# Optimization experiments

Measured on AMD Instinct MI355X. Metric: run time of the kernel, lower is better.

Reference implementation:

```python
import jax, jax.numpy as jnp
import numpy as np

B, T = 128, 100
DZ, DA, DU, K, DOBS, H = 64, 32, 8, 8, 16, 128
JITTER = 1e-4  # _safe_cholesky: sym + jitter*I, then first try adds 1.0*jitter*I again


def setup_inputs() -> dict:
    key = jax.random.key(0)
    ks = jax.random.split(key, 10)
    eye_z = jnp.eye(DZ, dtype=jnp.float32)
    # stable-ish per-component transition matrices
    A_mats = 0.9 * eye_z[None] + 0.05 * jax.random.normal(ks[0], (K, DZ, DZ), jnp.float32)
    B_mats = 0.1 * jax.random.normal(ks[1], (K, DZ, DU), jnp.float32)
    C_mats = 0.3 * jax.random.normal(ks[2], (K, DA, DZ), jnp.float32)
    a_seq = jax.random.normal(ks[3], (B, T, DA), jnp.float32)
    h_obs = jax.random.normal(ks[4], (B, DOBS), jnp.float32)
    u_seq = jax.random.normal(ks[5], (B, T, DU), jnp.float32)
    mask = jnp.ones((B, T), jnp.float32)
    a_0 = jnp.zeros((1, DA), jnp.float32)          # nn.Parameter a_0
    P_0 = 10.0 * eye_z                              # 10 * eye(dim_z)
    Q = 0.05 * eye_z                                # Q_std * eye(dim_z)
    R = 0.05 * jnp.eye(DA, dtype=jnp.float32)       # R_std * eye(dim_a)
    din = DA + DOBS + DU
    s = 1.0 / float(np.sqrt(H))
    W_ih = s * jax.random.normal(ks[6], (3 * H, din), jnp.float32)
    W_hh = s * jax.random.normal(ks[7], (3 * H, H), jnp.float32)
    b_ih = jnp.zeros((3 * H,), jnp.float32)
    b_hh = jnp.zeros((3 * H,), jnp.float32)
    W_out = s * jax.random.normal(ks[8], (K, H), jnp.float32)
    b_out = jnp.zeros((K,), jnp.float32)
    return dict(a_seq=a_seq, h_obs=h_obs, u_seq=u_seq, mask=mask,
                A_mats=A_mats, B_mats=B_mats, C_mats=C_mats,
                a_0=a_0, P_0=P_0, Q=Q, R=R,
                W_ih=W_ih, W_hh=W_hh, b_ih=b_ih, b_hh=b_hh,
                W_out=W_out, b_out=b_out, epoch=100)


def _sym(M):
    return 0.5 * (M + jnp.swapaxes(M, -1, -2))


def _gru_alpha(x, h, W_ih, W_hh, b_ih, b_hh, W_out, b_out):
    # GRU-cell alpha_net: mixture weights over K components
    gi = x @ W_ih.T + b_ih
    gh = h @ W_hh.T + b_hh
    ir, iz, inn = jnp.split(gi, 3, axis=-1)
    hr, hz, hn = jnp.split(gh, 3, axis=-1)
    r = jax.nn.sigmoid(ir + hr)
    zg = jax.nn.sigmoid(iz + hz)
    n = jnp.tanh(inn + r * hn)
    h_new = (1.0 - zg) * n + zg * h
    alpha = jax.nn.softmax(h_new @ W_out.T + b_out, axis=-1)
    return alpha, h_new


def _kalman_forward(a_seq, h_obs, u_seq, mask, A_mats, B_mats, C_mats,
                    a_0, P_0, Q, R, W_ih, W_hh, b_ih, b_hh, W_out, b_out):
    Bsz = a_seq.shape[0]
    I = jnp.eye(DZ, dtype=a_seq.dtype)

    def mix(alpha):
        A = jnp.einsum('bk,kij->bij', alpha, A_mats)
        Bc = jnp.einsum('bk,kij->bij', alpha, B_mats)
        C = jnp.einsum('bk,kij->bij', alpha, C_mats)
        return A, Bc, C

    def alpha_net(a, u, h):
        x = jnp.concatenate([a, h_obs, u], axis=-1)
        return _gru_alpha(x, h, W_ih, W_hh, b_ih, b_hh, W_out, b_out)

    gru_h = jnp.zeros((Bsz, H), a_seq.dtype)
    a_prev = jnp.broadcast_to(a_0, (Bsz, DA))
    alpha0, gru_h = alpha_net(a_prev, u_seq[:, 0], gru_h)
    A_k0, B_k0, C_k0 = mix(alpha0)

    z0 = jnp.zeros((Bsz, DZ), a_seq.dtype)
    P0 = jnp.broadcast_to(P_0, (Bsz, DZ, DZ))

    def step(carry, inp):
        z_prev, P, h, A_k, B_k, C_k = carry
        a_k, u_k, m_k = inp  # [B,da], [B,du], [B]
        mk = m_k[:, None]
        # predict with matrices chosen at previous step
        z = jnp.einsum('bij,bj->bi', A_k, z_prev) + jnp.einsum('bij,bj->bi', B_k, u_k)
        a_hat = jnp.einsum('bij,bj->bi', C_k, z)
        r_k = a_k - a_hat
        CP = jnp.einsum('bij,bjk->bik', C_k, P)                      # C P
        S = jnp.einsum('bik,bjk->bij', CP, C_k) + R                   # C P C^T + R
        # K = solve(S^T, C P^T)^T  (i.e. K = P C^T S^{-1})
        CPt = jnp.einsum('bij,bkj->bik', C_k, P)
        Kg = jnp.swapaxes(jnp.linalg.solve(jnp.swapaxes(S, -1, -2), CPt), -1, -2)
        Kg = Kg * m_k[:, None, None]
        IKC = I - jnp.einsum('bij,bjk->bik', Kg, C_k)
        # Joseph form update
        P_filt = (jnp.einsum('bij,bjk,blk->bil', IKC, P, IKC)
                  + jnp.einsum('bij,jk,blk->bil', Kg, R, Kg))
        P_filt = _sym(P_filt)
        z_mean = z + jnp.einsum('bij,bj->bi', Kg, r_k)
        L = jnp.linalg.cholesky(_sym(P_filt) + 2.0 * JITTER * I)      # safe cholesky
        z_filt = z_mean                                               # dist.mean
        a_filt = jnp.einsum('bij,bj->bi', C_k, z_filt)
        a_k_hat = mk * a_k + (1.0 - mk) * a_filt
        C_old = C_k
        alpha, h = alpha_net(a_k_hat, u_k, h)
        A_n, B_n, C_n = mix(alpha)
        z_pred = (jnp.einsum('bij,bj->bi', A_n, z_filt)
                  + jnp.einsum('bij,bj->bi', B_n, u_k))
        a_pred = jnp.einsum('bij,bj->bi', C_n, z_pred)
        P_pred = _sym(jnp.einsum('bij,bjk,blk->bil', A_n, P_filt, A_n) + Q)
        carry = (z_filt, P_pred, h, A_n, B_n, C_n)
        out = (z_filt, P_filt, z_pred, P_pred, alpha, a_filt, a_pred,
               S, z_mean, L, A_n, B_n, C_old)
        return carry, out

    xs = (jnp.swapaxes(a_seq, 0, 1), jnp.swapaxes(u_seq, 0, 1), jnp.swapaxes(mask, 0, 1))
    _, outs = jax.lax.scan(step, (z0, P0, gru_h, A_k0, B_k0, C_k0), xs)
    # scan outputs are [T, B, ...] -> [B, T, ...]
    (z_filt, P_filt, z_pred, P_pred, alpha_seq, a_filt, a_pred,
     S_pred, z_means, z_scale_tril, A_seq, B_seq, C_seq) = jax.tree.map(
        lambda x: jnp.swapaxes(x, 0, 1), outs)
    return (z_filt, P_filt, z_pred, a_filt, a_pred, P_pred, alpha_seq,
            A_seq, B_seq, C_seq, z_means, z_scale_tril, S_pred)


def reference(a_seq, h_obs, u_seq, mask, A_mats, B_mats, C_mats,
              a_0, P_0, Q, R, W_ih, W_hh, b_ih, b_hh, W_out, b_out, epoch):
    # epoch >= warmup/burn-in thresholds (all 0), so no detach branches apply
    return _kalman_forward(a_seq, h_obs, u_seq, mask, A_mats, B_mats, C_mats,
                           a_0, P_0, Q, R, W_ih, W_hh, b_ih, b_hh, W_out, b_out)
```

## Files before the change

### kernel.cpp

```cpp
#include <hip/hip_runtime.h>

typedef float f4 __attribute__((ext_vector_type(4)));

#define NT 256
#define BB 128
#define BT 100
#define DZc 64
#define DAc 32
#define DUc 8
#define KMIX 8
#define DOBSc 16
#define HG 128
#define DINc 56

#define O_ZFILT   0LL
#define O_PFILT   819200LL
#define O_ZPRED   53248000LL
#define O_AFILT   54067200LL
#define O_APRED   54476800LL
#define O_PPRED   54886400LL
#define O_ALPHA   107315200LL
#define O_ASEQ    107417600LL
#define O_BSEQ    159846400LL
#define O_CSEQ    166400000LL
#define O_ZMEAN   192614400LL
#define O_LTRIL   193433600LL
#define O_SPRED   245862400LL

__device__ __forceinline__ float dot4(f4 a, f4 b) {
    return a[0]*b[0] + a[1]*b[1] + a[2]*b[2] + a[3]*b[3];
}

struct SMem {
    float P[DZc][68];
    float A[DZc][68];
    float AT[DZc][68];
    float Wk[DZc][68];
    float Qm[DZc][68];
    float C[DAc][68];
    float CP[DAc][68];
    float Xm[DAc][68];
    float S[DAc][33];
    float Rm[DAc][33];
    float dinv[DAc];
    float Bm[DZc][8];
    float z[DZc], zp[DZc], zn[DZc];
    float h[HG];
    float gh[3*HG], gi[3*HG];
    float x[64];
    float ak[DAc], rvec[DAc];
    float u[8];
    float lg[8];
    float mk;
};

template<bool EMIT>
__device__ __forceinline__ void mix_apply(SMem& s, int tid, size_t bt, const float* al8,
    const float* __restrict__ A_mats, const float* __restrict__ B_mats,
    const float* __restrict__ C_mats, float* __restrict__ out)
{
    const f4* A4 = (const f4*)A_mats;
    const f4* B4 = (const f4*)B_mats;
    const f4* C4 = (const f4*)C_mats;
    #pragma unroll 2
    for (int e = 0; e < 4; ++e) {
        int i4 = tid + e*256;
        f4 acc = {0.f,0.f,0.f,0.f};
        #pragma unroll
        for (int k = 0; k < 8; ++k) acc += al8[k] * A4[k*1024 + i4];
        int row = i4 >> 4, cb = (i4 & 15) * 4;
        *(f4*)&s.A[row][cb] = acc;
        s.AT[cb][row] = acc[0]; s.AT[cb+1][row] = acc[1];
        s.AT[cb+2][row] = acc[2]; s.AT[cb+3][row] = acc[3];
        if (EMIT) *(f4*)&out[O_ASEQ + bt*4096 + (size_t)i4*4] = acc;
    }
    if (tid < 128) {
        int i4 = tid;
        f4 acc = {0.f,0.f,0.f,0.f};
        #pragma unroll
        for (int k = 0; k < 8; ++k) acc += al8[k] * B4[k*128 + i4];
        *(f4*)&s.Bm[i4>>1][(i4&1)*4] = acc;
        if (EMIT) *(f4*)&out[O_BSEQ + bt*512 + (size_t)i4*4] = acc;
    }
    #pragma unroll 1
    for (int e = 0; e < 2; ++e) {
        int i4 = tid + e*256;
        f4 acc = {0.f,0.f,0.f,0.f};
        #pragma unroll
        for (int k = 0; k < 8; ++k) acc += al8[k] * C4[k*512 + i4];
        *(f4*)&s.C[i4>>4][(i4&15)*4] = acc;
    }
}

__global__ void __launch_bounds__(NT, 1)
kalman_seq(const float* __restrict__ a_seq, const float* __restrict__ h_obs,
           const float* __restrict__ u_seq, const float* __restrict__ mask,
           const float* __restrict__ A_mats, const float* __restrict__ B_mats,
           const float* __restrict__ C_mats, const float* __restrict__ a_0,
           const float* __restrict__ P_0, const float* __restrict__ Q,
           const float* __restrict__ R, const float* __restrict__ W_ih,
           const float* __restrict__ W_hh, const float* __restrict__ b_ih,
           const float* __restrict__ b_hh, const float* __restrict__ W_out,
           const float* __restrict__ b_out, float* __restrict__ out)
{
    __shared__ SMem s;
    const int b = blockIdx.x;
    const int tid = threadIdx.x;
    const int r4 = (tid >> 4) << 2;
    const int c4 = (tid & 15) << 2;

    for (int idx = tid; idx < DZc*DZc; idx += NT) {
        s.P[idx >> 6][idx & 63]  = P_0[idx];
        s.Qm[idx >> 6][idx & 63] = Q[idx];
    }
    for (int idx = tid; idx < DAc*DAc; idx += NT) s.Rm[idx >> 5][idx & 31] = R[idx];
    if (tid < HG) s.h[tid] = 0.f;
    if (tid < DZc) s.z[tid] = 0.f;
    if (tid < DAc)                 s.x[tid] = a_0[tid];
    else if (tid < DAc + DOBSc)    s.x[tid] = h_obs[b*DOBSc + (tid - DAc)];
    else if (tid < DINc)           s.x[tid] = u_seq[(size_t)b*BT*DUc + (tid - DAc - DOBSc)];
    __syncthreads();

    for (int g = tid; g < 3*HG; g += NT) {
        const float* wi = W_ih + (size_t)g * DINc;
        f4 ai = {0.f,0.f,0.f,0.f};
        #pragma unroll 7
        for (int q = 0; q < 14; ++q) ai += *(const f4*)(wi + q*4) * *(const f4*)&s.x[q*4];
        s.gi[g] = ai[0]+ai[1]+ai[2]+ai[3] + b_ih[g];
        s.gh[g] = b_hh[g];
    }
    __syncthreads();
    if (tid < HG) {
        float r  = 1.f / (1.f + expf(-(s.gi[tid] + s.gh[tid])));
        float zg = 1.f / (1.f + expf(-(s.gi[HG+tid] + s.gh[HG+tid])));
        float n  = tanhf(s.gi[2*HG+tid] + r * s.gh[2*HG+tid]);
        s.h[tid] = (1.f - zg) * n;
    }
    __syncthreads();
    if (tid < KMIX) {
        const float* wo = W_out + tid * HG;
        f4 acc = {0.f,0.f,0.f,0.f};
        #pragma unroll 8
        for (int q = 0; q < 32; ++q) acc += *(const f4*)(wo + q*4) * *(const f4*)&s.h[q*4];
        s.lg[tid] = acc[0]+acc[1]+acc[2]+acc[3] + b_out[tid];
    }
    __syncthreads();
    {
        float lg[8];
        #pragma unroll
        for (int k = 0; k < 8; ++k) lg[k] = s.lg[k];
        float mx = lg[0];
        #pragma unroll
        for (int k = 1; k < 8; ++k) mx = fmaxf(mx, lg[k]);
        float al[8]; float sum = 0.f;
        #pragma unroll
        for (int k = 0; k < 8; ++k) { al[k] = expf(lg[k] - mx); sum += al[k]; }
        float rs = 1.f / sum;
        #pragma unroll
        for (int k = 0; k < 8; ++k) al[k] *= rs;
        mix_apply<false>(s, tid, 0, al, A_mats, B_mats, C_mats, out);
    }
    __syncthreads();

    for (int t = 0; t < BT; ++t) {
        const size_t bt = (size_t)b * BT + t;

        if (tid < 64) {
            float acc = 0.f;
            #pragma unroll 8
            for (int k = 0; k < DZc; ++k) acc += s.AT[k][tid] * s.z[k];
            const float* up = u_seq + bt*DUc;
            #pragma unroll
            for (int q = 0; q < DUc; ++q) acc += s.Bm[tid][q] * up[q];
            s.zp[tid] = acc;
        } else if (tid < 96) {
            float av = a_seq[bt*DAc + (tid-64)];
            s.ak[tid-64] = av;
            s.x[tid-64] = av;
        } else if (tid < 104) {
            float uv = u_seq[bt*DUc + (tid-96)];
            s.u[tid-96] = uv; s.x[48 + (tid-96)] = uv;
        } else if (tid == 104) {
            s.mk = mask[bt];
        }
        __syncthreads();
        const float mkv = s.mk;
        const bool mk1 = (mkv == 1.0f);

        {
            const int r = tid >> 3;
            const int c8 = (tid & 7) * 8;
            f4 acc0 = {0.f,0.f,0.f,0.f}, acc1 = {0.f,0.f,0.f,0.f};
            #pragma unroll 4
            for (int k4 = 0; k4 < 16; ++k4) {
                f4 cr = *(const f4*)&s.C[r][k4*4];
                #pragma unroll
                for (int kk = 0; kk < 4; ++kk) {
                    float cv = cr[kk];
                    acc0 += cv * *(const f4*)&s.P[k4*4+kk][c8];
                    acc1 += cv * *(const f4*)&s.P[k4*4+kk][c8+4];
                }
            }
            *(f4*)&s.CP[r][c8]   = acc0;
            *(f4*)&s.CP[r][c8+4] = acc1;
        }
        if (tid < DAc) {
            float acc = 0.f;
            #pragma unroll 4
            for (int k4 = 0; k4 < 16; ++k4)
                acc += dot4(*(const f4*)&s.C[tid][k4*4], *(const f4*)&s.zp[k4*4]);
            s.rvec[tid] = s.ak[tid] - acc;
        }
        __syncthreads();

        {
            const int r = tid >> 3;
            const int cb = (tid & 7) * 4;
            f4 acc = {0.f,0.f,0.f,0.f};
            #pragma unroll 4
            for (int k4 = 0; k4 < 16; ++k4) {
                f4 a = *(const f4*)&s.CP[r][k4*4];
                #pragma unroll
                for (int j = 0; j < 4; ++j)
                    acc[j] += dot4(a, *(const f4*)&s.C[cb+j][k4*4]);
            }
            f4 rm = {s.Rm[r][cb], s.Rm[r][cb+1], s.Rm[r][cb+2], s.Rm[r][cb+3]};
            f4 v = acc + rm;
            s.S[r][cb] = v[0]; s.S[r][cb+1] = v[1]; s.S[r][cb+2] = v[2]; s.S[r][cb+3] = v[3];
            *(f4*)&out[O_SPRED + bt*1024 + (size_t)r*32 + cb] = v;
        }
        __syncthreads();

        if (tid < 64) {
            const int lane = tid;
            const int l = lane & 31, par = lane >> 5;
            for (int k = 0; k < 31; ++k) {
                __threadfence_block();
                float dv = 1.0f / s.S[k][k];
                if (lane == k) s.dinv[k] = dv;
                if (l > k) {
                    float f = s.S[l][k] * dv;
                    for (int j = k + 1 + par; j <= l; j += 2)
                        s.S[l][j] -= f * s.S[j][k];
                }
            }
            __threadfence_block();
            if (lane == 31) s.dinv[31] = 1.0f / s.S[31][31];
            __threadfence_block();
            #pragma unroll 8
            for (int r = 0; r < 32; ++r) s.Xm[r][lane] = s.CP[r][lane];
            s.Xm[0][lane] *= s.dinv[0];
            #pragma unroll 1
            for (int r = 1; r < 32; ++r) {
                float acc = s.Xm[r][lane];
                #pragma unroll 4
                for (int k = 0; k < r; ++k) acc -= s.S[r][k] * s.Xm[k][lane];
                s.Xm[r][lane] = s.dinv[r] * acc;
            }
            #pragma unroll 1
            for (int r = 30; r >= 0; --r) {
                float acc = 0.f;
                #pragma unroll 4
                for (int k = r+1; k < 32; ++k) acc += s.S[k][r] * s.Xm[k][lane];
                s.Xm[r][lane] -= s.dinv[r] * acc;
            }
            float accz = 0.f;
            #pragma unroll 4
            for (int r = 0; r < 32; ++r) accz += s.Xm[r][lane] * s.rvec[r];
            s.zn[lane] = s.zp[lane] + mkv * accz;
        } else {
            #pragma unroll 1
            for (int g = tid - 64; g < 3*HG; g += 192) {
                const float* wi = W_ih + (size_t)g * DINc;
                const float* wh = W_hh + (size_t)g * HG;
                f4 ai = {0.f,0.f,0.f,0.f}, ah = {0.f,0.f,0.f,0.f};
                #pragma unroll 7
                for (int q = 0; q < 14; ++q) ai += *(const f4*)(wi + q*4) * *(const f4*)&s.x[q*4];
                #pragma unroll 8
                for (int q = 0; q < 32; ++q) ah += *(const f4*)(wh + q*4) * *(const f4*)&s.h[q*4];
                s.gi[g] = ai[0]+ai[1]+ai[2]+ai[3] + b_ih[g];
                s.gh[g] = ah[0]+ah[1]+ah[2]+ah[3] + b_hh[g];
            }
        }
        __syncthreads();

        {
            const float coef = (mkv*mkv - 2.f*mkv) * 0.5f;
            f4 acc0 = {0.f,0.f,0.f,0.f}, acc1 = {0.f,0.f,0.f,0.f};
            f4 acc2 = {0.f,0.f,0.f,0.f}, acc3 = {0.f,0.f,0.f,0.f};
            #pragma unroll 4
            for (int l = 0; l < DAc; ++l) {
                f4 cpc = *(const f4*)&s.CP[l][c4];
                f4 xc  = *(const f4*)&s.Xm[l][c4];
                f4 cpr = *(const f4*)&s.CP[l][r4];
                f4 xr  = *(const f4*)&s.Xm[l][r4];
                acc0 += xr[0]*cpc + cpr[0]*xc;
                acc1 += xr[1]*cpc + cpr[1]*xc;
                acc2 += xr[2]*cpc + cpr[2]*xc;
                acc3 += xr[3]*cpc + cpr[3]*xc;
            }
            #pragma unroll
            for (int i = 0; i < 4; ++i) {
                const int row = r4 + i;
                f4 g = (i==0) ? acc0 : (i==1) ? acc1 : (i==2) ? acc2 : acc3;
                f4 p = *(const f4*)&s.P[row][c4];
                f4 v = p + coef * g;
                *(f4*)&s.P[row][c4] = v;
                *(f4*)&out[O_PFILT + bt*4096 + (size_t)row*64 + c4] = v;
            }
        }
        if (tid < DZc) {
            float v = s.zn[tid];
            out[O_ZFILT + bt*DZc + tid] = v;
            out[O_ZMEAN + bt*DZc + tid] = v;
            s.z[tid] = v;
        }
        if (tid < DAc) {
            float acc = 0.f;
            #pragma unroll 4
            for (int k4 = 0; k4 < 16; ++k4)
                acc += dot4(*(const f4*)&s.C[tid][k4*4], *(const f4*)&s.zn[k4*4]);
            out[O_AFILT + bt*DAc + tid] = acc;
            s.x[tid] = mkv * s.ak[tid] + (1.f - mkv) * acc;
        }
        #pragma unroll 1
        for (int e = 0; e < 2; ++e) {
            int i4 = tid + e*256;
            *(f4*)&out[O_CSEQ + bt*2048 + (size_t)i4*4] = *(const f4*)&s.C[i4>>4][(i4&15)*4];
        }
        if (mk1 && tid < HG) {
            float gi0 = s.gi[tid], gi1 = s.gi[HG+tid], gi2 = s.gi[2*HG+tid];
            float gh0 = s.gh[tid], gh1 = s.gh[HG+tid], gh2 = s.gh[2*HG+tid];
            float hold = s.h[tid];
            float r  = 1.f / (1.f + expf(-(gi0 + gh0)));
            float zg = 1.f / (1.f + expf(-(gi1 + gh1)));
            float n  = tanhf(gi2 + r * gh2);
            s.h[tid] = (1.f - zg) * n + zg * hold;
        }
        __syncthreads();

        if (!mk1) {
            for (int g = tid; g < 3*HG; g += NT) {
                const float* wi = W_ih + (size_t)g * DINc;
                f4 ai = {0.f,0.f,0.f,0.f};
                #pragma unroll 7
                for (int q = 0; q < 14; ++q) ai += *(const f4*)(wi + q*4) * *(const f4*)&s.x[q*4];
                s.gi[g] = ai[0]+ai[1]+ai[2]+ai[3] + b_ih[g];
            }
            __syncthreads();
            if (tid < HG) {
                float gi0 = s.gi[tid], gi1 = s.gi[HG+tid], gi2 = s.gi[2*HG+tid];
                float gh0 = s.gh[tid], gh1 = s.gh[HG+tid], gh2 = s.gh[2*HG+tid];
                float hold = s.h[tid];
                float r  = 1.f / (1.f + expf(-(gi0 + gh0)));
                float zg = 1.f / (1.f + expf(-(gi1 + gh1)));
                float n  = tanhf(gi2 + r * gh2);
                s.h[tid] = (1.f - zg) * n + zg * hold;
            }
            __syncthreads();
        }

        if (tid < KMIX) {
            const float* wo = W_out + tid * HG;
            f4 acc = {0.f,0.f,0.f,0.f};
            #pragma unroll 8
            for (int q = 0; q < 32; ++q) acc += *(const f4*)(wo + q*4) * *(const f4*)&s.h[q*4];
            s.lg[tid] = acc[0]+acc[1]+acc[2]+acc[3] + b_out[tid];
        }
        __syncthreads();

        {
            float lg[8];
            #pragma unroll
            for (int k = 0; k < 8; ++k) lg[k] = s.lg[k];
            float mx = lg[0];
            #pragma unroll
            for (int k = 1; k < 8; ++k) mx = fmaxf(mx, lg[k]);
            float al[8]; float sum = 0.f;
            #pragma unroll
            for (int k = 0; k < 8; ++k) { al[k] = expf(lg[k] - mx); sum += al[k]; }
            float rs = 1.f / sum;
            #pragma unroll
            for (int k = 0; k < 8; ++k) al[k] *= rs;
            if (tid < 8) out[O_ALPHA + bt*8 + tid] = al[tid];
            mix_apply<true>(s, tid, bt, al, A_mats, B_mats, C_mats, out);
        }
        __syncthreads();

        if (tid < DZc) {
            float acc = 0.f;
            #pragma unroll 4
            for (int k4 = 0; k4 < 16; ++k4)
                acc += dot4(*(const f4*)&s.A[tid][k4*4], *(const f4*)&s.z[k4*4]);
            acc += dot4(*(const f4*)&s.Bm[tid][0], *(const f4*)&s.u[0]);
            acc += dot4(*(const f4*)&s.Bm[tid][4], *(const f4*)&s.u[4]);
            s.zp[tid] = acc;
            out[O_ZPRED + bt*DZc + tid] = acc;
        }
        {
            f4 acc[4] = {{0.f,0.f,0.f,0.f},{0.f,0.f,0.f,0.f},{0.f,0.f,0.f,0.f},{0.f,0.f,0.f,0.f}};
            #pragma unroll 2
            for (int k4 = 0; k4 < 16; ++k4) {
                #pragma unroll
                for (int kk = 0; kk < 4; ++kk) {
                    f4 bv = *(const f4*)&s.P[k4*4+kk][c4];
                    #pragma unroll
                    for (int i = 0; i < 4; ++i)
                        acc[i] += s.A[r4+i][k4*4+kk] * bv;
                }
            }
            #pragma unroll
            for (int i = 0; i < 4; ++i)
                *(f4*)&s.Wk[r4+i][c4] = acc[i];
        }
        __syncthreads();

        {
            f4 acc[4] = {{0.f,0.f,0.f,0.f},{0.f,0.f,0.f,0.f},{0.f,0.f,0.f,0.f},{0.f,0.f,0.f,0.f}};
            #pragma unroll 2
            for (int k4 = 0; k4 < 16; ++k4) {
                #pragma unroll
                for (int kk = 0; kk < 4; ++kk) {
                    f4 av = *(const f4*)&s.AT[k4*4+kk][c4];
                    #pragma unroll
                    for (int i = 0; i < 4; ++i)
                        acc[i] += s.Wk[r4+i][k4*4+kk] * av;
                }
            }
            #pragma unroll
            for (int i = 0; i < 4; ++i) {
                const int row = r4 + i;
                f4 q = *(const f4*)&s.Qm[row][c4];
                f4 v = acc[i] + q;
                *(f4*)&s.P[row][c4] = v;
                *(f4*)&out[O_PPRED + bt*4096 + (size_t)row*64 + c4] = v;
            }
        }
        if (tid < DAc) {
            float acc = 0.f;
            #pragma unroll 4
            for (int k4 = 0; k4 < 16; ++k4)
                acc += dot4(*(const f4*)&s.C[tid][k4*4], *(const f4*)&s.zp[k4*4]);
            out[O_APRED + bt*DAc + tid] = acc;
        }
        __syncthreads();
    }
}

__global__ void __launch_bounds__(64)
chol_batch(float* __restrict__ out)
{
    __shared__ float M[DZc][65];
    __shared__ float sd[DZc];
    const size_t bt = blockIdx.x;
    const int lane = threadIdx.x;
    const float* src = out + O_PFILT + bt*4096;
    #pragma unroll 4
    for (int e = 0; e < 16; ++e) {
        int i4 = lane + e*64;
        f4 v = *(const f4*)(src + (size_t)i4*4);
        int row = i4 >> 4, cb = (i4 & 15) * 4;
        M[row][cb] = v[0]; M[row][cb+1] = v[1]; M[row][cb+2] = v[2]; M[row][cb+3] = v[3];
    }
    __syncthreads();
    M[lane][lane] += 2.0e-4f;
    __syncthreads();
    for (int k = 0; k < DZc; ++k) {
        __threadfence_block();
        float mkk = M[k][k];
        if (lane == k) sd[k] = sqrtf(mkk);
        if (lane > k) {
            float f = M[lane][k] / mkk;
            for (int j = k + 1; j <= lane; ++j)
                M[lane][j] -= f * M[j][k];
        }
    }
    __threadfence_block();
    for (int k = 0; k < lane; ++k) M[lane][k] /= sd[k];
    M[lane][lane] = sd[lane];
    for (int k = lane + 1; k < DZc; ++k) M[lane][k] = 0.f;
    __syncthreads();
    float* dst = out + O_LTRIL + bt*4096;
    #pragma unroll 4
    for (int e = 0; e < 16; ++e) {
        int i4 = lane + e*64;
        int row = i4 >> 4, cb = (i4 & 15) * 4;
        f4 v = {M[row][cb], M[row][cb+1], M[row][cb+2], M[row][cb+3]};
        *(f4*)(dst + (size_t)i4*4) = v;
    }
}

extern "C" void kernel_launch(void* const* d_in, const int* in_sizes, int n_in,
                              void* d_out, int out_size, void* d_ws, size_t ws_size,
                              hipStream_t stream) {
    const float* a_seq  = (const float*)d_in[0];
    const float* h_obs  = (const float*)d_in[1];
    const float* u_seq  = (const float*)d_in[2];
    const float* mask   = (const float*)d_in[3];
    const float* A_mats = (const float*)d_in[4];
    const float* B_mats = (const float*)d_in[5];
    const float* C_mats = (const float*)d_in[6];
    const float* a_0    = (const float*)d_in[7];
    const float* P_0    = (const float*)d_in[8];
    const float* Q      = (const float*)d_in[9];
    const float* R      = (const float*)d_in[10];
    const float* W_ih   = (const float*)d_in[11];
    const float* W_hh   = (const float*)d_in[12];
    const float* b_ih   = (const float*)d_in[13];
    const float* b_hh   = (const float*)d_in[14];
    const float* W_out  = (const float*)d_in[15];
    const float* b_out  = (const float*)d_in[16];
    float* out = (float*)d_out;

    kalman_seq<<<dim3(BB), dim3(NT), 0, stream>>>(a_seq, h_obs, u_seq, mask,
        A_mats, B_mats, C_mats, a_0, P_0, Q, R, W_ih, W_hh, b_ih, b_hh, W_out, b_out, out);
    chol_batch<<<dim3(BB*BT), dim3(64), 0, stream>>>(out);
}
```

Before: 7.501 ms.

## Invert S via Gauss-Jordan, transpose C, shuffle logits, pack four Cholesky blocks per CTA

```diff
diff --git a/kernel.cpp b/kernel.cpp
--- a/kernel.cpp
+++ b/kernel.cpp
@@ -38,11 +38,12 @@
     float Wk[DZc][68];
     float Qm[DZc][68];
     float C[DAc][68];
+    float CT[DZc][36];
     float CP[DAc][68];
     float Xm[DAc][68];
     float S[DAc][33];
     float Rm[DAc][33];
-    float dinv[DAc];
+    float w[DAc];
     float Bm[DZc][8];
     float z[DZc], zp[DZc], zn[DZc];
     float h[HG];
@@ -88,7 +89,10 @@
         f4 acc = {0.f,0.f,0.f,0.f};
         #pragma unroll
         for (int k = 0; k < 8; ++k) acc += al8[k] * C4[k*512 + i4];
-        *(f4*)&s.C[i4>>4][(i4&15)*4] = acc;
+        int row = i4 >> 4, cb = (i4 & 15) * 4;
+        *(f4*)&s.C[row][cb] = acc;
+        s.CT[cb][row] = acc[0]; s.CT[cb+1][row] = acc[1];
+        s.CT[cb+2][row] = acc[2]; s.CT[cb+3][row] = acc[3];
     }
 }
 
@@ -221,8 +225,8 @@
             for (int k4 = 0; k4 < 16; ++k4) {
                 f4 a = *(const f4*)&s.CP[r][k4*4];
                 #pragma unroll
-                for (int j = 0; j < 4; ++j)
-                    acc[j] += dot4(a, *(const f4*)&s.C[cb+j][k4*4]);
+                for (int kk = 0; kk < 4; ++kk)
+                    acc += a[kk] * *(const f4*)&s.CT[k4*4+kk][cb];
             }
             f4 rm = {s.Rm[r][cb], s.Rm[r][cb+1], s.Rm[r][cb+2], s.Rm[r][cb+3]};
             f4 v = acc + rm;
@@ -232,42 +236,30 @@
         __syncthreads();
 
         if (tid < 64) {
-            const int lane = tid;
-            const int l = lane & 31, par = lane >> 5;
-            for (int k = 0; k < 31; ++k) {
+            const int l = tid & 31;
+            const int half = (tid >> 5) * 16;
+            for (int k = 0; k < DAc; ++k) {
                 __threadfence_block();
-                float dv = 1.0f / s.S[k][k];
-                if (lane == k) s.dinv[k] = dv;
-                if (l > k) {
-                    float f = s.S[l][k] * dv;
-                    for (int j = k + 1 + par; j <= l; j += 2)
-                        s.S[l][j] -= f * s.S[j][k];
+                float piv = 1.0f / s.S[k][k];
+                float flp = s.S[l][k] * piv;
+                const bool isk = (l == k);
+                #pragma unroll 4
+                for (int jj = 0; jj < 16; ++jj) {
+                    int j = half + jj;
+                    float skj = s.S[k][j];
+                    float newv;
+                    if (j == k) newv = isk ? piv : -flp;
+                    else        newv = isk ? piv * skj : s.S[l][j] - flp * skj;
+                    s.S[l][j] = newv;
                 }
             }
             __threadfence_block();
-            if (lane == 31) s.dinv[31] = 1.0f / s.S[31][31];
-            __threadfence_block();
-            #pragma unroll 8
-            for (int r = 0; r < 32; ++r) s.Xm[r][lane] = s.CP[r][lane];
-            s.Xm[0][lane] *= s.dinv[0];
-            #pragma unroll 1
-            for (int r = 1; r < 32; ++r) {
-                float acc = s.Xm[r][lane];
-                #pragma unroll 4
-                for (int k = 0; k < r; ++k) acc -= s.S[r][k] * s.Xm[k][lane];
-                s.Xm[r][lane] = s.dinv[r] * acc;
-            }
-            #pragma unroll 1
-            for (int r = 30; r >= 0; --r) {
+            if (tid < DAc) {
                 float acc = 0.f;
                 #pragma unroll 4
-                for (int k = r+1; k < 32; ++k) acc += s.S[k][r] * s.Xm[k][lane];
-                s.Xm[r][lane] -= s.dinv[r] * acc;
-            }
-            float accz = 0.f;
-            #pragma unroll 4
-            for (int r = 0; r < 32; ++r) accz += s.Xm[r][lane] * s.rvec[r];
-            s.zn[lane] = s.zp[lane] + mkv * accz;
+                for (int j = 0; j < DAc; ++j) acc += s.S[tid][j] * s.rvec[j];
+                s.w[tid] = acc;
+            }
         } else {
             #pragma unroll 1
             for (int g = tid - 64; g < 3*HG; g += 192) {
@@ -285,6 +277,27 @@
         __syncthreads();
 
         {
+            const int r = tid >> 3;
+            const int c8 = (tid & 7) * 8;
+            f4 x0 = {0.f,0.f,0.f,0.f}, x1 = {0.f,0.f,0.f,0.f};
+            #pragma unroll 4
+            for (int j = 0; j < DAc; ++j) {
+                float sv = s.S[r][j];
+                x0 += sv * *(const f4*)&s.CP[j][c8];
+                x1 += sv * *(const f4*)&s.CP[j][c8+4];
+            }
+            *(f4*)&s.Xm[r][c8]   = x0;
+            *(f4*)&s.Xm[r][c8+4] = x1;
+        }
+        if (tid < 64) {
+            float acc = 0.f;
+            #pragma unroll 4
+            for (int r = 0; r < DAc; ++r) acc += s.CP[r][tid] * s.w[r];
+            s.zn[tid] = s.zp[tid] + mkv * acc;
+        }
+        __syncthreads();
+
+        {
             const float coef = (mkv*mkv - 2.f*mkv) * 0.5f;
             f4 acc0 = {0.f,0.f,0.f,0.f}, acc1 = {0.f,0.f,0.f,0.f};
             f4 acc2 = {0.f,0.f,0.f,0.f}, acc3 = {0.f,0.f,0.f,0.f};
@@ -360,19 +373,19 @@
             __syncthreads();
         }
 
-        if (tid < KMIX) {
-            const float* wo = W_out + tid * HG;
-            f4 acc = {0.f,0.f,0.f,0.f};
-            #pragma unroll 8
-            for (int q = 0; q < 32; ++q) acc += *(const f4*)(wo + q*4) * *(const f4*)&s.h[q*4];
-            s.lg[tid] = acc[0]+acc[1]+acc[2]+acc[3] + b_out[tid];
-        }
-        __syncthreads();
-
-        {
+        {
+            const int lane = tid & 63;
+            const int g = lane >> 3;
+            const int cb = (lane & 7) * 16;
+            f4 a4 = {0.f,0.f,0.f,0.f};
+            #pragma unroll
+            for (int q = 0; q < 4; ++q)
+                a4 += *(const f4*)(W_out + (size_t)g*HG + cb + q*4) * *(const f4*)&s.h[cb + q*4];
+            float acc = a4[0]+a4[1]+a4[2]+a4[3];
+            acc += __shfl_xor(acc, 1); acc += __shfl_xor(acc, 2); acc += __shfl_xor(acc, 4);
             float lg[8];
             #pragma unroll
-            for (int k = 0; k < 8; ++k) lg[k] = s.lg[k];
+            for (int k = 0; k < 8; ++k) lg[k] = __shfl(acc, k*8) + b_out[k];
             float mx = lg[0];
             #pragma unroll
             for (int k = 1; k < 8; ++k) mx = fmaxf(mx, lg[k]);
@@ -387,11 +400,10 @@
         }
         __syncthreads();
 
-        if (tid < DZc) {
+        if (tid < 64) {
             float acc = 0.f;
-            #pragma unroll 4
-            for (int k4 = 0; k4 < 16; ++k4)
-                acc += dot4(*(const f4*)&s.A[tid][k4*4], *(const f4*)&s.z[k4*4]);
+            #pragma unroll 8
+            for (int k = 0; k < DZc; ++k) acc += s.AT[k][tid] * s.z[k];
             acc += dot4(*(const f4*)&s.Bm[tid][0], *(const f4*)&s.u[0]);
             acc += dot4(*(const f4*)&s.Bm[tid][4], *(const f4*)&s.u[4]);
             s.zp[tid] = acc;
@@ -401,12 +413,15 @@
             f4 acc[4] = {{0.f,0.f,0.f,0.f},{0.f,0.f,0.f,0.f},{0.f,0.f,0.f,0.f},{0.f,0.f,0.f,0.f}};
             #pragma unroll 2
             for (int k4 = 0; k4 < 16; ++k4) {
+                f4 ar0 = *(const f4*)&s.A[r4+0][k4*4];
+                f4 ar1 = *(const f4*)&s.A[r4+1][k4*4];
+                f4 ar2 = *(const f4*)&s.A[r4+2][k4*4];
+                f4 ar3 = *(const f4*)&s.A[r4+3][k4*4];
                 #pragma unroll
                 for (int kk = 0; kk < 4; ++kk) {
                     f4 bv = *(const f4*)&s.P[k4*4+kk][c4];
-                    #pragma unroll
-                    for (int i = 0; i < 4; ++i)
-                        acc[i] += s.A[r4+i][k4*4+kk] * bv;
+                    acc[0] += ar0[kk] * bv; acc[1] += ar1[kk] * bv;
+                    acc[2] += ar2[kk] * bv; acc[3] += ar3[kk] * bv;
                 }
             }
             #pragma unroll
@@ -419,12 +434,15 @@
             f4 acc[4] = {{0.f,0.f,0.f,0.f},{0.f,0.f,0.f,0.f},{0.f,0.f,0.f,0.f},{0.f,0.f,0.f,0.f}};
             #pragma unroll 2
             for (int k4 = 0; k4 < 16; ++k4) {
+                f4 w0 = *(const f4*)&s.Wk[r4+0][k4*4];
+                f4 w1 = *(const f4*)&s.Wk[r4+1][k4*4];
+                f4 w2 = *(const f4*)&s.Wk[r4+2][k4*4];
+                f4 w3 = *(const f4*)&s.Wk[r4+3][k4*4];
                 #pragma unroll
                 for (int kk = 0; kk < 4; ++kk) {
                     f4 av = *(const f4*)&s.AT[k4*4+kk][c4];
-                    #pragma unroll
-                    for (int i = 0; i < 4; ++i)
-                        acc[i] += s.Wk[r4+i][k4*4+kk] * av;
+                    acc[0] += w0[kk] * av; acc[1] += w1[kk] * av;
+                    acc[2] += w2[kk] * av; acc[3] += w3[kk] * av;
                 }
             }
             #pragma unroll
@@ -447,45 +465,47 @@
     }
 }
 
-__global__ void __launch_bounds__(64)
+__global__ void __launch_bounds__(256)
 chol_batch(float* __restrict__ out)
 {
-    __shared__ float M[DZc][65];
-    __shared__ float sd[DZc];
-    const size_t bt = blockIdx.x;
-    const int lane = threadIdx.x;
+    __shared__ float M[4][DZc][65];
+    __shared__ float sd[4][DZc];
+    const int w = threadIdx.x >> 6;
+    const int lane = threadIdx.x & 63;
+    const size_t bt = (size_t)blockIdx.x * 4 + w;
+    float (*Mw)[65] = M[w];
+    float* sdw = sd[w];
     const float* src = out + O_PFILT + bt*4096;
     #pragma unroll 4
     for (int e = 0; e < 16; ++e) {
         int i4 = lane + e*64;
         f4 v = *(const f4*)(src + (size_t)i4*4);
         int row = i4 >> 4, cb = (i4 & 15) * 4;
-        M[row][cb] = v[0]; M[row][cb+1] = v[1]; M[row][cb+2] = v[2]; M[row][cb+3] = v[3];
-    }
-    __syncthreads();
-    M[lane][lane] += 2.0e-4f;
-    __syncthreads();
+        Mw[row][cb] = v[0]; Mw[row][cb+1] = v[1]; Mw[row][cb+2] = v[2]; Mw[row][cb+3] = v[3];
+    }
+    __threadfence_block();
+    Mw[lane][lane] += 2.0e-4f;
     for (int k = 0; k < DZc; ++k) {
         __threadfence_block();
-        float mkk = M[k][k];
-        if (lane == k) sd[k] = sqrtf(mkk);
+        float mkk = Mw[k][k];
+        if (lane == k) sdw[k] = sqrtf(mkk);
         if (lane > k) {
-            float f = M[lane][k] / mkk;
+            float f = Mw[lane][k] / mkk;
             for (int j = k + 1; j <= lane; ++j)
-                M[lane][j] -= f * M[j][k];
+                Mw[lane][j] -= f * Mw[j][k];
         }
     }
     __threadfence_block();
-    for (int k = 0; k < lane; ++k) M[lane][k] /= sd[k];
-    M[lane][lane] = sd[lane];
-    for (int k = lane + 1; k < DZc; ++k) M[lane][k] = 0.f;
-    __syncthreads();
+    for (int k = 0; k < lane; ++k) Mw[lane][k] /= sdw[k];
+    Mw[lane][lane] = sdw[lane];
+    for (int k = lane + 1; k < DZc; ++k) Mw[lane][k] = 0.f;
+    __threadfence_block();
     float* dst = out + O_LTRIL + bt*4096;
     #pragma unroll 4
     for (int e = 0; e < 16; ++e) {
         int i4 = lane + e*64;
         int row = i4 >> 4, cb = (i4 & 15) * 4;
-        f4 v = {M[row][cb], M[row][cb+1], M[row][cb+2], M[row][cb+3]};
+        f4 v = {Mw[row][cb], Mw[row][cb+1], Mw[row][cb+2], Mw[row][cb+3]};
         *(f4*)(dst + (size_t)i4*4) = v;
     }
 }
@@ -514,5 +534,5 @@
 
     kalman_seq<<<dim3(BB), dim3(NT), 0, stream>>>(a_seq, h_obs, u_seq, mask,
         A_mats, B_mats, C_mats, a_0, P_0, Q, R, W_ih, W_hh, b_ih, b_hh, W_out, b_out, out);
-    chol_batch<<<dim3(BB*BT), dim3(64), 0, stream>>>(out);
+    chol_batch<<<dim3(BB*BT/4), dim3(256), 0, stream>>>(out);
 }
```

Measured after the change: 7.777 ms. 1.04x slower.
